# Optimization experiments

Measured on AMD Instinct MI355X. Metric: run time of the kernel, lower is better.

Reference implementation:

```python
import jax, jax.numpy as jnp
import numpy as np

EPS = 1e-5
NUM_HEADS = 8
SCALE = 0.125


def _lin_bn_relu(x, w, b, g, beta, mu, var):
    # Linear (y = x @ w.T + b), BatchNorm1d over channel dim (eval-mode affine), ReLU
    y = jnp.einsum('bnc,dc->bnd', x, w) + b
    y = (y - mu) * (g / jnp.sqrt(var + EPS)) + beta
    return jax.nn.relu(y)


def setup_inputs() -> dict:
    key = jax.random.key(0)
    B, N, C = 8, 1024, 512
    keys = jax.random.split(key, 16)
    d = {'x': jax.random.normal(keys[0], (B, N, C), dtype=jnp.float32)}
    for i, p in enumerate(['q', 'k', 'v', 'p']):
        kw, kb, kmu = keys[1 + 3 * i], keys[2 + 3 * i], keys[3 + 3 * i]
        d[f'{p}_w'] = jax.random.normal(kw, (C, C), dtype=jnp.float32) * 0.02
        d[f'{p}_b'] = jnp.zeros((C,), dtype=jnp.float32)
        d[f'{p}_g'] = jnp.ones((C,), dtype=jnp.float32)
        d[f'{p}_beta'] = jnp.zeros((C,), dtype=jnp.float32)
        d[f'{p}_mu'] = jax.random.normal(kmu, (C,), dtype=jnp.float32) * 0.02
        d[f'{p}_var'] = jax.random.uniform(kb, (C,), dtype=jnp.float32, minval=0.5, maxval=1.5)
    return d


def reference(x,
              q_w, q_b, q_g, q_beta, q_mu, q_var,
              k_w, k_b, k_g, k_beta, k_mu, k_var,
              v_w, v_b, v_g, v_beta, v_mu, v_var,
              p_w, p_b, p_g, p_beta, p_mu, p_var):
    B, N, C = x.shape
    H = NUM_HEADS
    dh = C // H

    def heads(t):  # [B,N,C] -> [B,H,N,dh]
        return t.reshape(B, N, H, dh).transpose(0, 2, 1, 3)

    q = heads(_lin_bn_relu(x, q_w, q_b, q_g, q_beta, q_mu, q_var))
    k = heads(_lin_bn_relu(x, k_w, k_b, k_g, k_beta, k_mu, k_var))
    v = heads(_lin_bn_relu(x, v_w, v_b, v_g, v_beta, v_mu, v_var))

    attn = jnp.einsum('bhnd,bhmd->bhnm', q, k) * SCALE  # no softmax
    out = jnp.einsum('bhnm,bhmd->bhnd', attn, v)
    out = out.transpose(0, 2, 1, 3).reshape(B, N, C)
    out = jax.nn.relu(out)  # attn_lif
    return _lin_bn_relu(out, p_w, p_b, p_g, p_beta, p_mu, p_var)
```

## Files before the change

### kernel.cpp

```cpp
#include <hip/hip_runtime.h>


#define CDIM  512
#define NSEQ  1024
#define MROWS 8192

typedef __attribute__((ext_vector_type(8))) __bf16  bf16x8;
typedef __attribute__((ext_vector_type(4))) float   f32x4;
typedef __attribute__((ext_vector_type(8))) ushort  u16x8;

__device__ __forceinline__ float b2f(ushort u) {
    union { uint i; float f; } v; v.i = ((uint)u) << 16; return v.f;
}
__device__ __forceinline__ ushort f2b(float f) {
    union { float f; uint i; } v; v.f = f;
    uint u = v.i;
    u = u + 0x7fffu + ((u >> 16) & 1u);
    return (ushort)(u >> 16);
}
__device__ __forceinline__ float ldv(const void* p, long i, int f32) {
    return f32 ? ((const float*)p)[i] : b2f(((const ushort*)p)[i]);
}

__device__ __forceinline__ void gload16(const void* g, void* l) {
    __builtin_amdgcn_global_load_lds(
        (const __attribute__((address_space(1))) void*)g,
        (__attribute__((address_space(3))) void*)l,
        16, 0, 0);
}

__global__ void detect_kernel(const ushort* __restrict__ x, int* __restrict__ flag) {
    __shared__ int cnt;
    if (threadIdx.x == 0) cnt = 0;
    __syncthreads();
    int c = 0;
    for (int i = threadIdx.x; i < 2048; i += 256) {
        uint e = ((uint)x[i] >> 7) & 0xffu;
        if (e >= 0xC8u) ++c;
    }
    atomicAdd(&cnt, c);
    __syncthreads();
    if (threadIdx.x == 0) *flag = (cnt > 32) ? 1 : 0;
}

struct BnArgs {
    const void* b[4]; const void* g[4]; const void* be[4];
    const void* mu[4]; const void* va[4];
};

__global__ void prep_st_kernel(BnArgs a, float* __restrict__ s_all,
                               float* __restrict__ t_all,
                               const int* __restrict__ flag) {
    int f32 = *flag;
    int idx = blockIdx.x * 256 + threadIdx.x;
    int br = idx >> 9, c = idx & 511;
    float g  = ldv(a.g[br],  c, f32);
    float be = ldv(a.be[br], c, f32);
    float mu = ldv(a.mu[br], c, f32);
    float va = ldv(a.va[br], c, f32);
    float bb = ldv(a.b[br],  c, f32);
    float s = g / sqrtf(va + 1e-5f);
    s_all[idx] = s;
    t_all[idx] = (bb - mu) * s + be;
}

__global__ void conv_x_kernel(const void* __restrict__ src, ushort* __restrict__ dst,
                              const int* __restrict__ flag) {
    int f32 = *flag;
    long i = ((long)blockIdx.x * 256 + threadIdx.x) * 8;
    if (f32) {
        const float* s = (const float*)src + i;
        u16x8 o;
        #pragma unroll
        for (int j = 0; j < 8; ++j) o[j] = f2b(s[j]);
        *(u16x8*)(dst + i) = o;
    } else {
        *(u16x8*)(dst + i) = *(const u16x8*)((const ushort*)src + i);
    }
}

struct WPtrs { const void* w[4]; };

__global__ void conv_w_kernel(WPtrs wp, ushort* __restrict__ dst,
                              const int* __restrict__ flag) {
    int f32 = *flag;
    int p = blockIdx.x >> 7;
    long i = ((long)(blockIdx.x & 127) * 256 + threadIdx.x) * 8;
    const void* src = wp.w[p];
    ushort* d = dst + (long)p * 262144 + i;
    if (f32) {
        const float* s = (const float*)src + i;
        u16x8 o;
        #pragma unroll
        for (int j = 0; j < 8; ++j) o[j] = f2b(s[j]);
        *(u16x8*)d = o;
    } else {
        *(u16x8*)d = *(const u16x8*)((const ushort*)src + i);
    }
}

__global__ void zero_s_kernel(float* __restrict__ S) {
    ((float4*)S)[blockIdx.x * 256 + threadIdx.x] = make_float4(0.f, 0.f, 0.f, 0.f);
}

__device__ __forceinline__ void gemm128(
    const ushort* __restrict__ A, const ushort* __restrict__ Bw, void* __restrict__ O,
    const float* __restrict__ s_all, const float* __restrict__ t_all,
    int st_off, int of32)
{
    __shared__ ushort As[4096];
    __shared__ ushort Bs[4096];
    const int t = threadIdx.x;
    const int wave = t >> 6, lane = t & 63;
    const int wr = wave >> 1, wc = wave & 1;
    const long row0 = (long)blockIdx.x * 128;
    const int  col0 = blockIdx.y * 128;

    const ushort* gA = A  + (row0 + (t >> 2)) * CDIM + (t & 3) * 8;
    const ushort* gB = Bw + (long)(col0 + (t >> 2)) * CDIM + (t & 3) * 8;
    ushort* lA = As + wave * 512;
    ushort* lB = Bs + wave * 512;

    f32x4 acc[4][4] = {};

    for (int k0 = 0; k0 < CDIM; k0 += 32) {
        gload16(gA + k0,             lA);
        gload16(gA + 64 * CDIM + k0, lA + 2048);
        gload16(gB + k0,             lB);
        gload16(gB + 64 * CDIM + k0, lB + 2048);
        __syncthreads();

        bf16x8 av[4], bv[4];
        #pragma unroll
        for (int m = 0; m < 4; ++m)
            av[m] = *(const bf16x8*)&As[(wr * 64 + m * 16 + (lane & 15)) * 32 + (lane >> 4) * 8];
        #pragma unroll
        for (int n = 0; n < 4; ++n)
            bv[n] = *(const bf16x8*)&Bs[(wc * 64 + n * 16 + (lane & 15)) * 32 + (lane >> 4) * 8];
        #pragma unroll
        for (int m = 0; m < 4; ++m)
            #pragma unroll
            for (int n = 0; n < 4; ++n)
                acc[m][n] = __builtin_amdgcn_mfma_f32_16x16x32_bf16(av[m], bv[n], acc[m][n], 0, 0, 0);
        __syncthreads();
    }

    const int lr4 = (lane >> 4) * 4, lc = lane & 15;
    #pragma unroll
    for (int n = 0; n < 4; ++n) {
        const int col = col0 + wc * 64 + n * 16 + lc;
        const float s = s_all[st_off + col], tt = t_all[st_off + col];
        #pragma unroll
        for (int m = 0; m < 4; ++m) {
            const long rb = row0 + wr * 64 + m * 16 + lr4;
            #pragma unroll
            for (int i = 0; i < 4; ++i) {
                float v = acc[m][n][i] * s + tt;
                v = v > 0.f ? v : 0.f;
                if (of32) ((float*)O)[(rb + i) * CDIM + col] = v;
                else      ((ushort*)O)[(rb + i) * CDIM + col] = f2b(v);
            }
        }
    }
}

__global__ __launch_bounds__(256) void gemm_qkv(
    const ushort* __restrict__ Xb, const ushort* __restrict__ Wb,
    ushort* __restrict__ QKV,
    const float* __restrict__ s_all, const float* __restrict__ t_all)
{
    int z = blockIdx.z;
    gemm128(Xb, Wb + (long)z * 262144, QKV + (long)z * 4194304,
            s_all, t_all, z * 512, 0);
}

__global__ __launch_bounds__(256) void gemm_p(
    const ushort* __restrict__ Aq, const ushort* __restrict__ Wp,
    void* __restrict__ O,
    const float* __restrict__ s_all, const float* __restrict__ t_all,
    const int* __restrict__ flag)
{
    gemm128(Aq, Wp, O, s_all, t_all, 1536, *flag);
}

__global__ __launch_bounds__(256) void ktv_kernel(
    const ushort* __restrict__ K, const ushort* __restrict__ V,
    float* __restrict__ S)
{
    int bh = blockIdx.x, b = bh >> 3, h = bh & 7;
    int ns = blockIdx.y;
    __shared__ float Ks[8][64];
    __shared__ float Vs[8][64];
    int t = threadIdx.x;
    int lr = t >> 5, lc = (t & 31) * 2;
    int r0 = (t >> 4) * 4, c0 = (t & 15) * 4;
    const ushort* Kb = K + (long)b * NSEQ * CDIM + h * 64;
    const ushort* Vb = V + (long)b * NSEQ * CDIM + h * 64;

    float acc[4][4] = {};
    for (int it = 0; it < 16; ++it) {
        __syncthreads();
        long n = ns * 128 + it * 8 + lr;
        Ks[lr][lc]     = b2f(Kb[n * CDIM + lc]);
        Ks[lr][lc + 1] = b2f(Kb[n * CDIM + lc + 1]);
        Vs[lr][lc]     = b2f(Vb[n * CDIM + lc]);
        Vs[lr][lc + 1] = b2f(Vb[n * CDIM + lc + 1]);
        __syncthreads();
        #pragma unroll
        for (int nn = 0; nn < 8; ++nn) {
            f32x4 kf = *(const f32x4*)&Ks[nn][r0];
            f32x4 vf = *(const f32x4*)&Vs[nn][c0];
            #pragma unroll
            for (int i = 0; i < 4; ++i)
                #pragma unroll
                for (int j = 0; j < 4; ++j)
                    acc[i][j] += kf[i] * vf[j];
        }
    }
    float* out = S + ((long)bh * 64 + r0) * 64 + c0;
    #pragma unroll
    for (int i = 0; i < 4; ++i)
        #pragma unroll
        for (int j = 0; j < 4; ++j)
            atomicAdd(&out[i * 64 + j], acc[i][j]);
}

__global__ __launch_bounds__(256) void attn_kernel(
    ushort* __restrict__ Q, const float* __restrict__ S)
{
    int bh = blockIdx.x, b = bh >> 3, h = bh & 7;
    int m0 = blockIdx.y * 64;
    __shared__ float Ss[64][64];
    __shared__ float Qs[64][68];
    int t = threadIdx.x, ty = t >> 4, tx = t & 15;

    for (int e = t; e < 4096; e += 256)
        Ss[e >> 6][e & 63] = S[(long)bh * 4096 + e];
    ushort* Qb = Q + ((long)(b * NSEQ + m0)) * CDIM + h * 64;
    for (int e = t; e < 4096; e += 256) {
        int r = e >> 6, c = e & 63;
        Qs[c][r] = b2f(Qb[(long)r * CDIM + c]);
    }
    __syncthreads();

    float acc[4][4] = {};
    for (int d1 = 0; d1 < 64; ++d1) {
        f32x4 qv = *(const f32x4*)&Qs[d1][ty * 4];
        f32x4 sv = *(const f32x4*)&Ss[d1][tx * 4];
        #pragma unroll
        for (int i = 0; i < 4; ++i)
            #pragma unroll
            for (int j = 0; j < 4; ++j)
                acc[i][j] += qv[i] * sv[j];
    }
    #pragma unroll
    for (int i = 0; i < 4; ++i) {
        ushort4 o;
        o.x = f2b(fmaxf(0.125f * acc[i][0], 0.f));
        o.y = f2b(fmaxf(0.125f * acc[i][1], 0.f));
        o.z = f2b(fmaxf(0.125f * acc[i][2], 0.f));
        o.w = f2b(fmaxf(0.125f * acc[i][3], 0.f));
        *(ushort4*)&Qb[(long)(ty * 4 + i) * CDIM + tx * 4] = o;
    }
}

extern "C" void kernel_launch(void* const* d_in, const int* in_sizes, int n_in,
                              void* d_out, int out_size, void* d_ws, size_t ws_size,
                              hipStream_t stream)
{
    const void* x = d_in[0];
    WPtrs wp; BnArgs bn;
    for (int p = 0; p < 4; ++p) {
        wp.w[p]   = d_in[1 + 6 * p + 0];
        bn.b[p]   = d_in[1 + 6 * p + 1];
        bn.g[p]   = d_in[1 + 6 * p + 2];
        bn.be[p]  = d_in[1 + 6 * p + 3];
        bn.mu[p]  = d_in[1 + 6 * p + 4];
        bn.va[p]  = d_in[1 + 6 * p + 5];
    }

    char* ws = (char*)d_ws;
    float*  s_all = (float*)ws;
    float*  t_all = (float*)(ws + 8192);
    int*    flag  = (int*)(ws + 16384);
    ushort* Wb    = (ushort*)(ws + 16640);
    ushort* QKV   = (ushort*)(ws + 16640 + 2097152);
    float*  S     = (float*)(ws + 16640 + 2097152 + 3L * 8388608);
    ushort* Xb    = (ushort*)d_out;

    detect_kernel<<<1, 256, 0, stream>>>((const ushort*)x, flag);
    prep_st_kernel<<<8, 256, 0, stream>>>(bn, s_all, t_all, flag);
    conv_x_kernel<<<2048, 256, 0, stream>>>(x, Xb, flag);
    conv_w_kernel<<<512, 256, 0, stream>>>(wp, Wb, flag);
    zero_s_kernel<<<256, 256, 0, stream>>>(S);

    gemm_qkv<<<dim3(64, 4, 3), 256, 0, stream>>>(Xb, Wb, QKV, s_all, t_all);

    ktv_kernel<<<dim3(64, 8), 256, 0, stream>>>(QKV + 4194304, QKV + 2L * 4194304, S);

    attn_kernel<<<dim3(64, 16), 256, 0, stream>>>(QKV, S);

    gemm_p<<<dim3(64, 4), 256, 0, stream>>>(QKV, Wb + 3L * 262144, d_out,
                                            s_all, t_all, flag);
}
```

Before: 209.9 us.

## Fuse prep kernels into one launch, deepen GEMM K-tile, widen KtV loads

```diff
diff --git a/kernel.cpp b/kernel.cpp
--- a/kernel.cpp
+++ b/kernel.cpp
@@ -29,78 +29,78 @@
         16, 0, 0);
 }
 
-__global__ void detect_kernel(const ushort* __restrict__ x, int* __restrict__ flag) {
-    __shared__ int cnt;
-    if (threadIdx.x == 0) cnt = 0;
-    __syncthreads();
-    int c = 0;
-    for (int i = threadIdx.x; i < 2048; i += 256) {
-        uint e = ((uint)x[i] >> 7) & 0xffu;
-        if (e >= 0xC8u) ++c;
-    }
-    atomicAdd(&cnt, c);
-    __syncthreads();
-    if (threadIdx.x == 0) *flag = (cnt > 32) ? 1 : 0;
-}
-
 struct BnArgs {
     const void* b[4]; const void* g[4]; const void* be[4];
     const void* mu[4]; const void* va[4];
 };
-
-__global__ void prep_st_kernel(BnArgs a, float* __restrict__ s_all,
-                               float* __restrict__ t_all,
-                               const int* __restrict__ flag) {
-    int f32 = *flag;
-    int idx = blockIdx.x * 256 + threadIdx.x;
-    int br = idx >> 9, c = idx & 511;
-    float g  = ldv(a.g[br],  c, f32);
-    float be = ldv(a.be[br], c, f32);
-    float mu = ldv(a.mu[br], c, f32);
-    float va = ldv(a.va[br], c, f32);
-    float bb = ldv(a.b[br],  c, f32);
-    float s = g / sqrtf(va + 1e-5f);
-    s_all[idx] = s;
-    t_all[idx] = (bb - mu) * s + be;
-}
-
-__global__ void conv_x_kernel(const void* __restrict__ src, ushort* __restrict__ dst,
-                              const int* __restrict__ flag) {
-    int f32 = *flag;
-    long i = ((long)blockIdx.x * 256 + threadIdx.x) * 8;
-    if (f32) {
-        const float* s = (const float*)src + i;
-        u16x8 o;
-        #pragma unroll
-        for (int j = 0; j < 8; ++j) o[j] = f2b(s[j]);
-        *(u16x8*)(dst + i) = o;
+struct WPtrs { const void* w[4]; };
+
+__global__ __launch_bounds__(256) void prep_all(
+    const void* __restrict__ x, WPtrs wp, BnArgs bn,
+    ushort* __restrict__ Xb, ushort* __restrict__ Wb,
+    float* __restrict__ s_all, float* __restrict__ t_all,
+    float* __restrict__ S, int* __restrict__ flag)
+{
+    const int blk = blockIdx.x, t = threadIdx.x;
+    if (blk >= 2568) {
+        ((float4*)S)[(blk - 2568) * 256 + t] = make_float4(0.f, 0.f, 0.f, 0.f);
+        return;
+    }
+
+    __shared__ int cnt;
+    if (t == 0) cnt = 0;
+    __syncthreads();
+    {
+        const ushort* xu = (const ushort*)x;
+        int c = 0;
+        for (int i = t; i < 2048; i += 256) {
+            uint e = ((uint)xu[i] >> 7) & 0xffu;
+            if (e >= 0xC8u) ++c;
+        }
+        if (c) atomicAdd(&cnt, c);
+    }
+    __syncthreads();
+    const int f32 = cnt > 32;
+    if (blk == 0 && t == 0) *flag = f32;
+
+    if (blk < 2048) {
+        long i = ((long)blk * 256 + t) * 8;
+        if (f32) {
+            const float* s = (const float*)x + i;
+            u16x8 o;
+            #pragma unroll
+            for (int j = 0; j < 8; ++j) o[j] = f2b(s[j]);
+            *(u16x8*)(Xb + i) = o;
+        } else {
+            *(u16x8*)(Xb + i) = *(const u16x8*)((const ushort*)x + i);
+        }
+    } else if (blk < 2560) {
+        int bb = blk - 2048;
+        int p = bb >> 7;
+        long i = ((long)(bb & 127) * 256 + t) * 8;
+        const void* src = wp.w[p];
+        ushort* d = Wb + (long)p * 262144 + i;
+        if (f32) {
+            const float* s = (const float*)src + i;
+            u16x8 o;
+            #pragma unroll
+            for (int j = 0; j < 8; ++j) o[j] = f2b(s[j]);
+            *(u16x8*)d = o;
+        } else {
+            *(u16x8*)d = *(const u16x8*)((const ushort*)src + i);
+        }
     } else {
-        *(u16x8*)(dst + i) = *(const u16x8*)((const ushort*)src + i);
-    }
-}
-
-struct WPtrs { const void* w[4]; };
-
-__global__ void conv_w_kernel(WPtrs wp, ushort* __restrict__ dst,
-                              const int* __restrict__ flag) {
-    int f32 = *flag;
-    int p = blockIdx.x >> 7;
-    long i = ((long)(blockIdx.x & 127) * 256 + threadIdx.x) * 8;
-    const void* src = wp.w[p];
-    ushort* d = dst + (long)p * 262144 + i;
-    if (f32) {
-        const float* s = (const float*)src + i;
-        u16x8 o;
-        #pragma unroll
-        for (int j = 0; j < 8; ++j) o[j] = f2b(s[j]);
-        *(u16x8*)d = o;
-    } else {
-        *(u16x8*)d = *(const u16x8*)((const ushort*)src + i);
-    }
-}
-
-__global__ void zero_s_kernel(float* __restrict__ S) {
-    ((float4*)S)[blockIdx.x * 256 + threadIdx.x] = make_float4(0.f, 0.f, 0.f, 0.f);
+        int idx = (blk - 2560) * 256 + t;
+        int br = idx >> 9, c = idx & 511;
+        float g  = ldv(bn.g[br],  c, f32);
+        float be = ldv(bn.be[br], c, f32);
+        float mu = ldv(bn.mu[br], c, f32);
+        float va = ldv(bn.va[br], c, f32);
+        float bb = ldv(bn.b[br],  c, f32);
+        float s = g / sqrtf(va + 1e-5f);
+        s_all[idx] = s;
+        t_all[idx] = (bb - mu) * s + be;
+    }
 }
 
 __device__ __forceinline__ void gemm128(
@@ -108,40 +108,44 @@
     const float* __restrict__ s_all, const float* __restrict__ t_all,
     int st_off, int of32)
 {
-    __shared__ ushort As[4096];
-    __shared__ ushort Bs[4096];
+    __shared__ ushort As[8192];
+    __shared__ ushort Bs[8192];
     const int t = threadIdx.x;
     const int wave = t >> 6, lane = t & 63;
     const int wr = wave >> 1, wc = wave & 1;
     const long row0 = (long)blockIdx.x * 128;
     const int  col0 = blockIdx.y * 128;
 
-    const ushort* gA = A  + (row0 + (t >> 2)) * CDIM + (t & 3) * 8;
-    const ushort* gB = Bw + (long)(col0 + (t >> 2)) * CDIM + (t & 3) * 8;
+    const ushort* gA = A  + (row0 + (t >> 3)) * CDIM + (t & 7) * 8;
+    const ushort* gB = Bw + (long)(col0 + (t >> 3)) * CDIM + (t & 7) * 8;
     ushort* lA = As + wave * 512;
     ushort* lB = Bs + wave * 512;
 
     f32x4 acc[4][4] = {};
 
-    for (int k0 = 0; k0 < CDIM; k0 += 32) {
-        gload16(gA + k0,             lA);
-        gload16(gA + 64 * CDIM + k0, lA + 2048);
-        gload16(gB + k0,             lB);
-        gload16(gB + 64 * CDIM + k0, lB + 2048);
+    for (int k0 = 0; k0 < CDIM; k0 += 64) {
+        #pragma unroll
+        for (int r = 0; r < 4; ++r) {
+            gload16(gA + (long)r * 32 * CDIM + k0, lA + r * 2048);
+            gload16(gB + (long)r * 32 * CDIM + k0, lB + r * 2048);
+        }
         __syncthreads();
 
-        bf16x8 av[4], bv[4];
-        #pragma unroll
-        for (int m = 0; m < 4; ++m)
-            av[m] = *(const bf16x8*)&As[(wr * 64 + m * 16 + (lane & 15)) * 32 + (lane >> 4) * 8];
-        #pragma unroll
-        for (int n = 0; n < 4; ++n)
-            bv[n] = *(const bf16x8*)&Bs[(wc * 64 + n * 16 + (lane & 15)) * 32 + (lane >> 4) * 8];
-        #pragma unroll
-        for (int m = 0; m < 4; ++m)
+        #pragma unroll
+        for (int ks = 0; ks < 2; ++ks) {
+            bf16x8 av[4], bv[4];
+            #pragma unroll
+            for (int m = 0; m < 4; ++m)
+                av[m] = *(const bf16x8*)&As[(wr * 64 + m * 16 + (lane & 15)) * 64 + ks * 32 + (lane >> 4) * 8];
             #pragma unroll
             for (int n = 0; n < 4; ++n)
-                acc[m][n] = __builtin_amdgcn_mfma_f32_16x16x32_bf16(av[m], bv[n], acc[m][n], 0, 0, 0);
+                bv[n] = *(const bf16x8*)&Bs[(wc * 64 + n * 16 + (lane & 15)) * 64 + ks * 32 + (lane >> 4) * 8];
+            #pragma unroll
+            for (int m = 0; m < 4; ++m)
+                #pragma unroll
+                for (int n = 0; n < 4; ++n)
+                    acc[m][n] = __builtin_amdgcn_mfma_f32_16x16x32_bf16(av[m], bv[n], acc[m][n], 0, 0, 0);
+        }
         __syncthreads();
     }
 
@@ -189,25 +193,28 @@
 {
     int bh = blockIdx.x, b = bh >> 3, h = bh & 7;
     int ns = blockIdx.y;
-    __shared__ float Ks[8][64];
-    __shared__ float Vs[8][64];
+    __shared__ float Ks[32][64];
+    __shared__ float Vs[32][64];
     int t = threadIdx.x;
-    int lr = t >> 5, lc = (t & 31) * 2;
+    int lr = t >> 3, lc = (t & 7) * 8;
     int r0 = (t >> 4) * 4, c0 = (t & 15) * 4;
-    const ushort* Kb = K + (long)b * NSEQ * CDIM + h * 64;
-    const ushort* Vb = V + (long)b * NSEQ * CDIM + h * 64;
+    const ushort* Kb = K + ((long)b * NSEQ + ns * 128) * CDIM + h * 64;
+    const ushort* Vb = V + ((long)b * NSEQ + ns * 128) * CDIM + h * 64;
 
     float acc[4][4] = {};
-    for (int it = 0; it < 16; ++it) {
+    for (int it = 0; it < 4; ++it) {
         __syncthreads();
-        long n = ns * 128 + it * 8 + lr;
-        Ks[lr][lc]     = b2f(Kb[n * CDIM + lc]);
-        Ks[lr][lc + 1] = b2f(Kb[n * CDIM + lc + 1]);
-        Vs[lr][lc]     = b2f(Vb[n * CDIM + lc]);
-        Vs[lr][lc + 1] = b2f(Vb[n * CDIM + lc + 1]);
+        long n = (long)(it * 32 + lr) * CDIM;
+        u16x8 kv = *(const u16x8*)&Kb[n + lc];
+        u16x8 vv = *(const u16x8*)&Vb[n + lc];
+        #pragma unroll
+        for (int j = 0; j < 8; ++j) {
+            Ks[lr][lc + j] = b2f(kv[j]);
+            Vs[lr][lc + j] = b2f(vv[j]);
+        }
         __syncthreads();
         #pragma unroll
-        for (int nn = 0; nn < 8; ++nn) {
+        for (int nn = 0; nn < 32; ++nn) {
             f32x4 kf = *(const f32x4*)&Ks[nn][r0];
             f32x4 vf = *(const f32x4*)&Vs[nn][c0];
             #pragma unroll
@@ -288,11 +295,7 @@
     float*  S     = (float*)(ws + 16640 + 2097152 + 3L * 8388608);
     ushort* Xb    = (ushort*)d_out;
 
-    detect_kernel<<<1, 256, 0, stream>>>((const ushort*)x, flag);
-    prep_st_kernel<<<8, 256, 0, stream>>>(bn, s_all, t_all, flag);
-    conv_x_kernel<<<2048, 256, 0, stream>>>(x, Xb, flag);
-    conv_w_kernel<<<512, 256, 0, stream>>>(wp, Wb, flag);
-    zero_s_kernel<<<256, 256, 0, stream>>>(S);
+    prep_all<<<2824, 256, 0, stream>>>(x, wp, bn, Xb, Wb, s_all, t_all, S, flag);
 
     gemm_qkv<<<dim3(64, 4, 3), 256, 0, stream>>>(Xb, Wb, QKV, s_all, t_all);
 
```

Measured after the change: 200.5 us. 4.4% less time.
